# Kernel tuning notes

Hardware: AMD Instinct MI355X
Metric: run time of the kernel (lower is better)

Reference implementation:

```python
import jax, jax.numpy as jnp
import numpy as np


def setup_inputs() -> dict:
    key = jax.random.key(0)
    k1, k2, k3, k4, k5 = jax.random.split(key, 5)
    B, Te, Td, De, Dd = 8, 256, 256, 512, 512
    return {
        "encoder_out_seq": jax.random.normal(k1, (B, Te, De), dtype=jnp.float32),
        "decoder_out_seq": jax.random.normal(k2, (B, Td, Dd), dtype=jnp.float32),
        "W_a": jax.random.normal(k3, (De, De), dtype=jnp.float32) * 0.05,
        "U_a": jax.random.normal(k4, (Dd, De), dtype=jnp.float32) * 0.05,
        "V_a": jax.random.normal(k5, (De, 1), dtype=jnp.float32) * 0.05,
    }


def reference(encoder_out_seq, decoder_out_seq, W_a, U_a, V_a):
    # Bahdanau additive attention, fully vectorized over decoder timesteps
    # (replaces the two sequential K.rnn scans in the original).
    Ws = jnp.einsum('bte,ef->btf', encoder_out_seq, W_a)   # [B,Te,De]
    Uh = jnp.einsum('bqd,df->bqf', decoder_out_seq, U_a)   # [B,Td,De]
    # scores[b,q,t] = tanh(Ws[b,t,:] + Uh[b,q,:]) . V_a
    scores = jnp.einsum('bqtf,f->bqt',
                        jnp.tanh(Ws[:, None, :, :] + Uh[:, :, None, :]),
                        V_a[:, 0])                          # [B,Td,Te]
    e = jax.nn.softmax(scores, axis=-1)                     # attention weights
    c = jnp.einsum('bqt,btf->bqf', e, encoder_out_seq)      # context vectors
    return (c, e)
```

## Files before the change

kernel.cpp:

```cpp
#include <hip/hip_runtime.h>

#define NB 8
#define TE 256
#define TD 256
#define DE 512
#define QT 4

#define K2SCALE 2.8853900817779268f

__global__ __launch_bounds__(512) void gemm2(
    const float* __restrict__ A0, const float* __restrict__ W0, float* __restrict__ C0,
    const float* __restrict__ A1, const float* __restrict__ W1, float* __restrict__ C1)
{
  constexpr int N = DE;
  constexpr int K = DE;
  constexpr int BM = 128, BN = 64, BK = 16;
  constexpr int BMp = BM + 4;
  constexpr int NS = K / BK;
  const float* A = blockIdx.z ? A1 : A0;
  const float* W = blockIdx.z ? W1 : W0;
  float*       C = blockIdx.z ? C1 : C0;
  const int tid = threadIdx.x;
  const int m0 = blockIdx.y * BM;
  const int n0 = blockIdx.x * BN;
  __shared__ __align__(16) float As[2][BK][BMp];
  __shared__ __align__(16) float Bs[2][BK][BN];
  const int am = tid >> 2, ak = (tid & 3) * 4;
  const int bk = tid >> 5, bn = (tid & 31) * 2;
  const int ty = tid >> 4, tx = tid & 15;

  float4 av = *(const float4*)(A + (size_t)(m0 + am) * K + ak);
  float2 bv = *(const float2*)(W + (size_t)bk * N + n0 + bn);
  As[0][ak + 0][am] = av.x; As[0][ak + 1][am] = av.y;
  As[0][ak + 2][am] = av.z; As[0][ak + 3][am] = av.w;
  *(float2*)&Bs[0][bk][bn] = bv;
  __syncthreads();

  float acc[4][4];
  #pragma unroll
  for (int i = 0; i < 4; ++i)
    #pragma unroll
    for (int j = 0; j < 4; ++j) acc[i][j] = 0.f;

  for (int s = 0; s < NS; ++s) {
    const int cur = s & 1;
    if (s + 1 < NS) {
      const int k0 = (s + 1) * BK;
      av = *(const float4*)(A + (size_t)(m0 + am) * K + k0 + ak);
      bv = *(const float2*)(W + (size_t)(k0 + bk) * N + n0 + bn);
    }
    #pragma unroll
    for (int k = 0; k < BK; ++k) {
      float4 a = *(const float4*)&As[cur][k][ty * 4];
      float4 b = *(const float4*)&Bs[cur][k][tx * 4];
      float aa[4] = {a.x, a.y, a.z, a.w};
      float bb[4] = {b.x, b.y, b.z, b.w};
      #pragma unroll
      for (int i = 0; i < 4; ++i)
        #pragma unroll
        for (int j = 0; j < 4; ++j)
          acc[i][j] = fmaf(aa[i], bb[j], acc[i][j]);
    }
    if (s + 1 < NS) {
      const int nxt = cur ^ 1;
      As[nxt][ak + 0][am] = av.x; As[nxt][ak + 1][am] = av.y;
      As[nxt][ak + 2][am] = av.z; As[nxt][ak + 3][am] = av.w;
      *(float2*)&Bs[nxt][bk][bn] = bv;
      __syncthreads();
    }
  }
  #pragma unroll
  for (int i = 0; i < 4; ++i) {
    float4 o = {__builtin_amdgcn_exp2f(acc[i][0] * K2SCALE),
                __builtin_amdgcn_exp2f(acc[i][1] * K2SCALE),
                __builtin_amdgcn_exp2f(acc[i][2] * K2SCALE),
                __builtin_amdgcn_exp2f(acc[i][3] * K2SCALE)};
    *(float4*)(C + (size_t)(m0 + ty * 4 + i) * N + n0 + tx * 4) = o;
  }
}

__global__ __launch_bounds__(512) void attn(
    const float* __restrict__ ws, const float* __restrict__ uh,
    const float* __restrict__ enc, const float* __restrict__ va,
    float* __restrict__ out_c, float* __restrict__ out_e)
{
  const int tid  = threadIdx.x;
  const int wave = tid >> 6;
  const int lane = tid & 63;
  const int b  = blockIdx.x >> 6;
  const int q0 = (blockIdx.x & 63) * QT;
  __shared__ float s_sc[QT][TE];
  __shared__ float red[3][QT][DE];
  const int fbase = lane * 8;

  float4 v0 = *(const float4*)(va + fbase);
  float4 v1 = *(const float4*)(va + fbase + 4);
  float v[8] = {v0.x, v0.y, v0.z, v0.w, v1.x, v1.y, v1.z, v1.w};

  float eu[QT][8];
  #pragma unroll
  for (int q = 0; q < QT; ++q) {
    const float* up = uh + (size_t)(b * TD + q0 + q) * DE + fbase;
    float4 u0 = *(const float4*)(up);
    float4 u1 = *(const float4*)(up + 4);
    eu[q][0] = u0.x; eu[q][1] = u0.y; eu[q][2] = u0.z; eu[q][3] = u0.w;
    eu[q][4] = u1.x; eu[q][5] = u1.y; eu[q][6] = u1.z; eu[q][7] = u1.w;
  }

  const int t0 = wave * 32;
  const float* wp = ws + (size_t)(b * TE + t0) * DE + fbase;
  float4 w0 = *(const float4*)(wp);
  float4 w1 = *(const float4*)(wp + 4);
  for (int t = t0; t < t0 + 32; ++t) {
    float cw[8] = {w0.x, w0.y, w0.z, w0.w, w1.x, w1.y, w1.z, w1.w};
    wp += DE;
    w0 = *(const float4*)(wp);
    w1 = *(const float4*)(wp + 4);
    float a[QT];
    #pragma unroll
    for (int q = 0; q < QT; ++q) {
      float A0 = fmaf(cw[0], eu[q][0], 1.f);
      float A1 = fmaf(cw[1], eu[q][1], 1.f);
      float A2 = fmaf(cw[2], eu[q][2], 1.f);
      float A3 = fmaf(cw[3], eu[q][3], 1.f);
      float B0 = fmaf(cw[4], eu[q][4], 1.f);
      float B1 = fmaf(cw[5], eu[q][5], 1.f);
      float B2 = fmaf(cw[6], eu[q][6], 1.f);
      float B3 = fmaf(cw[7], eu[q][7], 1.f);
      float n1 = fmaf(v[1], A0, v[0] * A1);
      float d1 = A0 * A1;
      float n2 = fmaf(v[3], A2, v[2] * A3);
      float d2 = A2 * A3;
      float N1 = fmaf(n2, d1, n1 * d2);
      float D1 = d1 * d2;
      float n3 = fmaf(v[5], B0, v[4] * B1);
      float d3 = B0 * B1;
      float n4 = fmaf(v[7], B2, v[6] * B3);
      float d4 = B2 * B3;
      float N2 = fmaf(n4, d3, n3 * d4);
      float D2 = d3 * d4;
      float s = N1 * __builtin_amdgcn_rcpf(D1);
      a[q] = fmaf(N2, __builtin_amdgcn_rcpf(D2), s);
    }
    {
      const bool h1 = lane & 1;
      float m0 = h1 ? a[1] : a[0], o0 = h1 ? a[0] : a[1];
      float m1 = h1 ? a[3] : a[2], o1 = h1 ? a[2] : a[3];
      float r0 = m0 + __shfl_xor(o0, 1, 64);
      float r1 = m1 + __shfl_xor(o1, 1, 64);
      const bool h2 = lane & 2;
      float mm = h2 ? r1 : r0, oo = h2 ? r0 : r1;
      float r = mm + __shfl_xor(oo, 2, 64);
      r += __shfl_xor(r, 4, 64);
      r += __shfl_xor(r, 8, 64);
      r += __shfl_xor(r, 16, 64);
      r += __shfl_xor(r, 32, 64);
      if (lane < QT) s_sc[lane][t] = -2.f * r;
    }
  }
  __syncthreads();

  if (wave < QT) {
    const int r = wave;
    float x[4];
    #pragma unroll
    for (int i = 0; i < 4; ++i) x[i] = s_sc[r][lane + 64 * i];
    float m = fmaxf(fmaxf(x[0], x[1]), fmaxf(x[2], x[3]));
    #pragma unroll
    for (int off = 32; off >= 1; off >>= 1) m = fmaxf(m, __shfl_xor(m, off, 64));
    const float L2E = 1.4426950408889634f;
    float ssum = 0.f;
    #pragma unroll
    for (int i = 0; i < 4; ++i) { x[i] = __builtin_amdgcn_exp2f((x[i] - m) * L2E); ssum += x[i]; }
    #pragma unroll
    for (int off = 32; off >= 1; off >>= 1) ssum += __shfl_xor(ssum, off, 64);
    float inv = 1.f / ssum;
    float* oe = out_e + (size_t)(b * TD + q0 + r) * TE;
    #pragma unroll
    for (int i = 0; i < 4; ++i) {
      float e = x[i] * inv;
      s_sc[r][lane + 64 * i] = e;
      oe[lane + 64 * i] = e;
    }
  }
  __syncthreads();

  {
    const int fgrp = tid >> 7;
    const int f4   = (tid & 127) * 4;
    float4 c[QT];
    #pragma unroll
    for (int q = 0; q < QT; ++q) c[q] = make_float4(0.f, 0.f, 0.f, 0.f);
    const float* eb = enc + (size_t)b * TE * DE + f4;
    const int tb = fgrp * 64;
    #pragma unroll 4
    for (int t = tb; t < tb + 64; ++t) {
      float4 ee = *(const float4*)(eb + (size_t)t * DE);
      #pragma unroll
      for (int q = 0; q < QT; ++q) {
        float w = s_sc[q][t];
        c[q].x = fmaf(w, ee.x, c[q].x);
        c[q].y = fmaf(w, ee.y, c[q].y);
        c[q].z = fmaf(w, ee.z, c[q].z);
        c[q].w = fmaf(w, ee.w, c[q].w);
      }
    }
    if (fgrp > 0) {
      #pragma unroll
      for (int q = 0; q < QT; ++q) *(float4*)&red[fgrp - 1][q][f4] = c[q];
    }
    __syncthreads();
    if (fgrp == 0) {
      #pragma unroll
      for (int q = 0; q < QT; ++q) {
        float4 r1 = *(const float4*)&red[0][q][f4];
        float4 r2 = *(const float4*)&red[1][q][f4];
        float4 r3 = *(const float4*)&red[2][q][f4];
        c[q].x += (r1.x + r2.x) + r3.x;
        c[q].y += (r1.y + r2.y) + r3.y;
        c[q].z += (r1.z + r2.z) + r3.z;
        c[q].w += (r1.w + r2.w) + r3.w;
        *(float4*)(out_c + (size_t)(b * TD + q0 + q) * DE + f4) = c[q];
      }
    }
  }
}

extern "C" void kernel_launch(void* const* d_in, const int* in_sizes, int n_in,
                              void* d_out, int out_size, void* d_ws, size_t ws_size,
                              hipStream_t stream) {
  const float* enc = (const float*)d_in[0];
  const float* dec = (const float*)d_in[1];
  const float* Wa  = (const float*)d_in[2];
  const float* Ua  = (const float*)d_in[3];
  const float* Va  = (const float*)d_in[4];
  float* out_c = (float*)d_out;
  float* out_e = out_c + (size_t)NB * TD * DE;
  float* ws = (float*)d_ws;
  float* uh = ws + (size_t)NB * TE * DE;

  gemm2<<<dim3(DE / 64, (NB * TE) / 128, 2), dim3(512), 0, stream>>>(
      enc, Wa, ws, dec, Ua, uh);
  attn<<<dim3(NB * (TD / QT)), dim3(512), 0, stream>>>(
      ws, uh, enc, Va, out_c, out_e);
}
```

Baseline: 80.99 us.

## Replace FP32 SIMT projection GEMM with split-bf16 MFMA GEMM

Replaces the scalar FP32 GEMM that computes both projections with a matrix-core GEMM using bf16x3-style splitting (hi*hi + lo*hi + hi*lo) to keep near-FP32 accuracy. Two new conversion kernels split the activations and weights into bf16 high/low parts, and transpose the weights to a K-contiguous layout. This trades the FMA-bound GEMM for three MFMAs per tile, at the cost of two extra kernel launches and extra memory traffic for the converted operands. The attention kernel is unchanged.

```diff
diff --git a/kernel.cpp b/kernel.cpp
--- a/kernel.cpp
+++ b/kernel.cpp
@@ -8,75 +8,156 @@
 
 #define K2SCALE 2.8853900817779268f
 
-__global__ __launch_bounds__(512) void gemm2(
-    const float* __restrict__ A0, const float* __restrict__ W0, float* __restrict__ C0,
-    const float* __restrict__ A1, const float* __restrict__ W1, float* __restrict__ C1)
+typedef short bf16x8 __attribute__((ext_vector_type(8)));
+typedef float f32x4 __attribute__((ext_vector_type(4)));
+typedef unsigned short u16x8 __attribute__((ext_vector_type(8)));
+
+static __device__ __forceinline__ unsigned short f2bf(float x) {
+  unsigned int u = __float_as_uint(x);
+  u += 0x7fffu + ((u >> 16) & 1u);
+  return (unsigned short)(u >> 16);
+}
+
+__global__ __launch_bounds__(256) void convA(
+    const float* __restrict__ s0, unsigned short* __restrict__ h0, unsigned short* __restrict__ l0,
+    const float* __restrict__ s1, unsigned short* __restrict__ h1, unsigned short* __restrict__ l1)
 {
-  constexpr int N = DE;
-  constexpr int K = DE;
-  constexpr int BM = 128, BN = 64, BK = 16;
-  constexpr int BMp = BM + 4;
-  constexpr int NS = K / BK;
-  const float* A = blockIdx.z ? A1 : A0;
-  const float* W = blockIdx.z ? W1 : W0;
-  float*       C = blockIdx.z ? C1 : C0;
-  const int tid = threadIdx.x;
-  const int m0 = blockIdx.y * BM;
-  const int n0 = blockIdx.x * BN;
-  __shared__ __align__(16) float As[2][BK][BMp];
-  __shared__ __align__(16) float Bs[2][BK][BN];
-  const int am = tid >> 2, ak = (tid & 3) * 4;
-  const int bk = tid >> 5, bn = (tid & 31) * 2;
-  const int ty = tid >> 4, tx = tid & 15;
-
-  float4 av = *(const float4*)(A + (size_t)(m0 + am) * K + ak);
-  float2 bv = *(const float2*)(W + (size_t)bk * N + n0 + bn);
-  As[0][ak + 0][am] = av.x; As[0][ak + 1][am] = av.y;
-  As[0][ak + 2][am] = av.z; As[0][ak + 3][am] = av.w;
-  *(float2*)&Bs[0][bk][bn] = bv;
+  const float* s = blockIdx.z ? s1 : s0;
+  unsigned short* H = blockIdx.z ? h1 : h0;
+  unsigned short* L = blockIdx.z ? l1 : l0;
+  size_t base = ((size_t)blockIdx.x * 256 + threadIdx.x) * 8;
+  float4 x0 = *(const float4*)(s + base);
+  float4 x1 = *(const float4*)(s + base + 4);
+  float xs[8] = {x0.x, x0.y, x0.z, x0.w, x1.x, x1.y, x1.z, x1.w};
+  u16x8 h, l;
+  #pragma unroll
+  for (int j = 0; j < 8; ++j) {
+    unsigned short hh = f2bf(xs[j]);
+    float hf = __uint_as_float((unsigned int)hh << 16);
+    h[j] = hh;
+    l[j] = f2bf(xs[j] - hf);
+  }
+  *(u16x8*)(H + base) = h;
+  *(u16x8*)(L + base) = l;
+}
+
+__global__ __launch_bounds__(256) void convB(
+    const float* __restrict__ w0, unsigned short* __restrict__ h0, unsigned short* __restrict__ l0,
+    const float* __restrict__ w1, unsigned short* __restrict__ h1, unsigned short* __restrict__ l1)
+{
+  const float* W = blockIdx.z ? w1 : w0;
+  unsigned short* H = blockIdx.z ? h1 : h0;
+  unsigned short* L = blockIdx.z ? l1 : l0;
+  __shared__ unsigned short sh[32][33], sl[32][33];
+  const int t = threadIdx.x;
+  const int k0 = blockIdx.y * 32, n0 = blockIdx.x * 32;
+  const int r = t >> 3, c = (t & 7) * 4;
+  float4 x = *(const float4*)(W + (size_t)(k0 + r) * DE + n0 + c);
+  float xs[4] = {x.x, x.y, x.z, x.w};
+  #pragma unroll
+  for (int j = 0; j < 4; ++j) {
+    unsigned short hh = f2bf(xs[j]);
+    float hf = __uint_as_float((unsigned int)hh << 16);
+    sh[r][c + j] = hh;
+    sl[r][c + j] = f2bf(xs[j] - hf);
+  }
   __syncthreads();
-
-  float acc[4][4];
-  #pragma unroll
-  for (int i = 0; i < 4; ++i)
-    #pragma unroll
-    for (int j = 0; j < 4; ++j) acc[i][j] = 0.f;
-
-  for (int s = 0; s < NS; ++s) {
-    const int cur = s & 1;
-    if (s + 1 < NS) {
-      const int k0 = (s + 1) * BK;
-      av = *(const float4*)(A + (size_t)(m0 + am) * K + k0 + ak);
-      bv = *(const float2*)(W + (size_t)(k0 + bk) * N + n0 + bn);
-    }
-    #pragma unroll
-    for (int k = 0; k < BK; ++k) {
-      float4 a = *(const float4*)&As[cur][k][ty * 4];
-      float4 b = *(const float4*)&Bs[cur][k][tx * 4];
-      float aa[4] = {a.x, a.y, a.z, a.w};
-      float bb[4] = {b.x, b.y, b.z, b.w};
-      #pragma unroll
-      for (int i = 0; i < 4; ++i)
-        #pragma unroll
-        for (int j = 0; j < 4; ++j)
-          acc[i][j] = fmaf(aa[i], bb[j], acc[i][j]);
-    }
-    if (s + 1 < NS) {
-      const int nxt = cur ^ 1;
-      As[nxt][ak + 0][am] = av.x; As[nxt][ak + 1][am] = av.y;
-      As[nxt][ak + 2][am] = av.z; As[nxt][ak + 3][am] = av.w;
-      *(float2*)&Bs[nxt][bk][bn] = bv;
-      __syncthreads();
-    }
-  }
-  #pragma unroll
-  for (int i = 0; i < 4; ++i) {
-    float4 o = {__builtin_amdgcn_exp2f(acc[i][0] * K2SCALE),
-                __builtin_amdgcn_exp2f(acc[i][1] * K2SCALE),
-                __builtin_amdgcn_exp2f(acc[i][2] * K2SCALE),
-                __builtin_amdgcn_exp2f(acc[i][3] * K2SCALE)};
-    *(float4*)(C + (size_t)(m0 + ty * 4 + i) * N + n0 + tx * 4) = o;
-  }
+  ushort4 oh, ol;
+  oh.x = sh[c + 0][r]; oh.y = sh[c + 1][r]; oh.z = sh[c + 2][r]; oh.w = sh[c + 3][r];
+  ol.x = sl[c + 0][r]; ol.y = sl[c + 1][r]; ol.z = sl[c + 2][r]; ol.w = sl[c + 3][r];
+  *(ushort4*)(H + (size_t)(n0 + r) * DE + k0 + c) = oh;
+  *(ushort4*)(L + (size_t)(n0 + r) * DE + k0 + c) = ol;
+}
+
+__global__ __launch_bounds__(256) void gemm_mfma(
+    const unsigned short* __restrict__ AH0, const unsigned short* __restrict__ AL0,
+    const unsigned short* __restrict__ BH0, const unsigned short* __restrict__ BL0,
+    float* __restrict__ C0,
+    const unsigned short* __restrict__ AH1, const unsigned short* __restrict__ AL1,
+    const unsigned short* __restrict__ BH1, const unsigned short* __restrict__ BL1,
+    float* __restrict__ C1)
+{
+  const unsigned short* AH = blockIdx.z ? AH1 : AH0;
+  const unsigned short* AL = blockIdx.z ? AL1 : AL0;
+  const unsigned short* BH = blockIdx.z ? BH1 : BH0;
+  const unsigned short* BL = blockIdx.z ? BL1 : BL0;
+  float*               C  = blockIdx.z ? C1  : C0;
+  const int tid  = threadIdx.x;
+  const int lane = tid & 63;
+  const int wave = tid >> 6;
+  const int wm = wave >> 1, wn = wave & 1;
+  const int g = lane >> 4, r16 = lane & 15;
+  const int m0 = blockIdx.y * 128, n0 = blockIdx.x * 64;
+  __shared__ __align__(16) unsigned short Ah[128][40], Al[128][40];
+  __shared__ __align__(16) unsigned short Bh[64][40],  Bl[64][40];
+  const int arow = tid >> 2;
+  const int apart = (tid & 3) * 8;
+
+  u16x8 pa0, pa1, pla0, pla1, pb, plb;
+#define LOADTILE(KT) do {                                                   \
+    const size_t ko = (size_t)(KT) * 32 + apart;                            \
+    const unsigned short* pa_ = AH + (size_t)(m0 + arow) * 512 + ko;        \
+    const unsigned short* pl_ = AL + (size_t)(m0 + arow) * 512 + ko;        \
+    const unsigned short* qb_ = BH + (size_t)(n0 + arow) * 512 + ko;        \
+    const unsigned short* ql_ = BL + (size_t)(n0 + arow) * 512 + ko;        \
+    pa0 = *(const u16x8*)pa_;  pa1 = *(const u16x8*)(pa_ + 64 * 512);       \
+    pla0 = *(const u16x8*)pl_; pla1 = *(const u16x8*)(pl_ + 64 * 512);      \
+    pb = *(const u16x8*)qb_;   plb = *(const u16x8*)ql_;                    \
+  } while (0)
+
+  f32x4 accm[4][2], acce[4][2];
+  #pragma unroll
+  for (int mt = 0; mt < 4; ++mt)
+    #pragma unroll
+    for (int nt = 0; nt < 2; ++nt) {
+      accm[mt][nt] = (f32x4){0.f, 0.f, 0.f, 0.f};
+      acce[mt][nt] = (f32x4){0.f, 0.f, 0.f, 0.f};
+    }
+
+  LOADTILE(0);
+  for (int kt = 0; kt < 16; ++kt) {
+    __syncthreads();
+    *(u16x8*)&Ah[arow][apart] = pa0;
+    *(u16x8*)&Ah[arow + 64][apart] = pa1;
+    *(u16x8*)&Al[arow][apart] = pla0;
+    *(u16x8*)&Al[arow + 64][apart] = pla1;
+    *(u16x8*)&Bh[arow][apart] = pb;
+    *(u16x8*)&Bl[arow][apart] = plb;
+    __syncthreads();
+    if (kt + 1 < 16) LOADTILE(kt + 1);
+    bf16x8 ah[4], al[4], bh[2], bl[2];
+    #pragma unroll
+    for (int mt = 0; mt < 4; ++mt) {
+      ah[mt] = *(const bf16x8*)&Ah[wm * 64 + mt * 16 + r16][g * 8];
+      al[mt] = *(const bf16x8*)&Al[wm * 64 + mt * 16 + r16][g * 8];
+    }
+    #pragma unroll
+    for (int nt = 0; nt < 2; ++nt) {
+      bh[nt] = *(const bf16x8*)&Bh[wn * 32 + nt * 16 + r16][g * 8];
+      bl[nt] = *(const bf16x8*)&Bl[wn * 32 + nt * 16 + r16][g * 8];
+    }
+    #pragma unroll
+    for (int mt = 0; mt < 4; ++mt)
+      #pragma unroll
+      for (int nt = 0; nt < 2; ++nt) {
+        accm[mt][nt] = __builtin_amdgcn_mfma_f32_16x16x32_bf16(ah[mt], bh[nt], accm[mt][nt], 0, 0, 0);
+        acce[mt][nt] = __builtin_amdgcn_mfma_f32_16x16x32_bf16(al[mt], bh[nt], acce[mt][nt], 0, 0, 0);
+        acce[mt][nt] = __builtin_amdgcn_mfma_f32_16x16x32_bf16(ah[mt], bl[nt], acce[mt][nt], 0, 0, 0);
+      }
+  }
+#undef LOADTILE
+
+  #pragma unroll
+  for (int mt = 0; mt < 4; ++mt)
+    #pragma unroll
+    for (int nt = 0; nt < 2; ++nt)
+      #pragma unroll
+      for (int j = 0; j < 4; ++j) {
+        float vsum = accm[mt][nt][j] + acce[mt][nt][j];
+        int row = m0 + wm * 64 + mt * 16 + g * 4 + j;
+        int col = n0 + wn * 32 + nt * 16 + r16;
+        C[(size_t)row * 512 + col] = __builtin_amdgcn_exp2f(vsum * K2SCALE);
+      }
 }
 
 __global__ __launch_bounds__(512) void attn(
@@ -236,11 +317,22 @@
   const float* Va  = (const float*)d_in[4];
   float* out_c = (float*)d_out;
   float* out_e = out_c + (size_t)NB * TD * DE;
+
   float* ws = (float*)d_ws;
-  float* uh = ws + (size_t)NB * TE * DE;
-
-  gemm2<<<dim3(DE / 64, (NB * TE) / 128, 2), dim3(512), 0, stream>>>(
-      enc, Wa, ws, dec, Ua, uh);
+  float* uh = ws + 1048576;
+  unsigned short* AHe = (unsigned short*)(uh + 1048576);
+  unsigned short* ALe = AHe + 1048576;
+  unsigned short* AHd = ALe + 1048576;
+  unsigned short* ALd = AHd + 1048576;
+  unsigned short* BHw = ALd + 1048576;
+  unsigned short* BLw = BHw + 262144;
+  unsigned short* BHu = BLw + 262144;
+  unsigned short* BLu = BHu + 262144;
+
+  convA<<<dim3(512, 1, 2), dim3(256), 0, stream>>>(enc, AHe, ALe, dec, AHd, ALd);
+  convB<<<dim3(16, 16, 2), dim3(256), 0, stream>>>(Wa, BHw, BLw, Ua, BHu, BLu);
+  gemm_mfma<<<dim3(8, 16, 2), dim3(256), 0, stream>>>(
+      AHe, ALe, BHw, BLw, ws, AHd, ALd, BHu, BLu, uh);
   attn<<<dim3(NB * (TD / QT)), dim3(512), 0, stream>>>(
       ws, uh, enc, Va, out_c, out_e);
 }
```

Result: faster. 76.97 us (-5.0%).

## Replace FP32 SIMT GEMM with split-bf16 MFMA GEMM using prepacked operands

Applied to the files above, without the earlier changes.

Adds a prep kernel that splits the encoder/decoder activations and both weight matrices into high and low bf16 parts, stored in an MFMA-fragment layout. A new GEMM does the projections with 16x16x32 bf16 MFMA, three products per tile (hi*hi, lo*hi, hi*lo), to keep near-FP32 accuracy. It also remaps block indices across XCDs and swaps batch/query order in the attention grid. The aim is to move the projection work off FP32 FMA onto matrix cores, at the cost of an extra launch and extra packed-buffer traffic.

```diff
diff --git a/kernel.cpp b/kernel.cpp
--- a/kernel.cpp
+++ b/kernel.cpp
@@ -8,75 +8,152 @@
 
 #define K2SCALE 2.8853900817779268f
 
-__global__ __launch_bounds__(512) void gemm2(
-    const float* __restrict__ A0, const float* __restrict__ W0, float* __restrict__ C0,
-    const float* __restrict__ A1, const float* __restrict__ W1, float* __restrict__ C1)
+typedef short bf16x8 __attribute__((ext_vector_type(8)));
+typedef float f32x4 __attribute__((ext_vector_type(4)));
+typedef unsigned short u16x8 __attribute__((ext_vector_type(8)));
+
+static __device__ __forceinline__ unsigned short f2bf(float x) {
+  unsigned int u = __float_as_uint(x);
+  u += 0x7fffu + ((u >> 16) & 1u);
+  return (unsigned short)(u >> 16);
+}
+
+__global__ __launch_bounds__(256) void prep(
+    const float* __restrict__ enc, const float* __restrict__ dec,
+    const float* __restrict__ Wa,  const float* __restrict__ Ua,
+    unsigned short* __restrict__ AHp, unsigned short* __restrict__ ALp,
+    unsigned short* __restrict__ BHp, unsigned short* __restrict__ BLp)
 {
-  constexpr int N = DE;
-  constexpr int K = DE;
-  constexpr int BM = 128, BN = 64, BK = 16;
-  constexpr int BMp = BM + 4;
-  constexpr int NS = K / BK;
-  const float* A = blockIdx.z ? A1 : A0;
-  const float* W = blockIdx.z ? W1 : W0;
-  float*       C = blockIdx.z ? C1 : C0;
-  const int tid = threadIdx.x;
-  const int m0 = blockIdx.y * BM;
-  const int n0 = blockIdx.x * BN;
-  __shared__ __align__(16) float As[2][BK][BMp];
-  __shared__ __align__(16) float Bs[2][BK][BN];
-  const int am = tid >> 2, ak = (tid & 3) * 4;
-  const int bk = tid >> 5, bn = (tid & 31) * 2;
-  const int ty = tid >> 4, tx = tid & 15;
-
-  float4 av = *(const float4*)(A + (size_t)(m0 + am) * K + ak);
-  float2 bv = *(const float2*)(W + (size_t)bk * N + n0 + bn);
-  As[0][ak + 0][am] = av.x; As[0][ak + 1][am] = av.y;
-  As[0][ak + 2][am] = av.z; As[0][ak + 3][am] = av.w;
-  *(float2*)&Bs[0][bk][bn] = bv;
-  __syncthreads();
-
-  float acc[4][4];
+  const int b = blockIdx.x;
+  const int t = threadIdx.x;
+  if (b < 1024) {
+    const int z  = b >> 9;
+    const int rb = b & 511;
+    const int row = rb * 4 + (t >> 6);
+    const int tk  = t & 63;
+    const int k0  = tk * 8;
+    const float* src = (z ? dec : enc) + (size_t)row * DE + k0;
+    float4 x0 = *(const float4*)(src);
+    float4 x1 = *(const float4*)(src + 4);
+    float xs[8] = {x0.x, x0.y, x0.z, x0.w, x1.x, x1.y, x1.z, x1.w};
+    u16x8 h, l;
+    #pragma unroll
+    for (int j = 0; j < 8; ++j) {
+      unsigned short hh = f2bf(xs[j]);
+      float hf = __uint_as_float((unsigned int)hh << 16);
+      h[j] = hh;
+      l[j] = f2bf(xs[j] - hf);
+    }
+    const int m_tile = row >> 4, r16 = row & 15;
+    const int k_tile = tk >> 2, g = tk & 3;
+    const int lane = g * 16 + r16;
+    const size_t dst = (((size_t)(z * 128 + m_tile) * 16 + k_tile) * 64 + lane) * 8;
+    *(u16x8*)(AHp + dst) = h;
+    *(u16x8*)(ALp + dst) = l;
+  } else {
+    if (t >= 128) return;
+    const int idx = b - 1024;
+    const int z  = idx >> 8;
+    const int ti = idx & 255;
+    const int k0 = (ti >> 4) * 32, n0 = (ti & 15) * 32;
+    const int sub = t >> 6, l = t & 63;
+    const int r16 = l & 15, g = l >> 4;
+    const int n = n0 + sub * 16 + r16;
+    const float* W = z ? Ua : Wa;
+    u16x8 h, lo;
+    #pragma unroll
+    for (int e = 0; e < 8; ++e) {
+      float x = W[(size_t)(k0 + g * 8 + e) * DE + n];
+      unsigned short hh = f2bf(x);
+      float hf = __uint_as_float((unsigned int)hh << 16);
+      h[e] = hh;
+      lo[e] = f2bf(x - hf);
+    }
+    const int n_tile = (ti & 15) * 2 + sub;
+    const int k_tile = ti >> 4;
+    const size_t dst = (((size_t)(z * 32 + n_tile) * 16 + k_tile) * 64 + l) * 8;
+    *(u16x8*)(BHp + dst) = h;
+    *(u16x8*)(BLp + dst) = lo;
+  }
+}
+
+__global__ __launch_bounds__(256) void gemm_pk(
+    const unsigned short* __restrict__ AH, const unsigned short* __restrict__ AL,
+    const unsigned short* __restrict__ BH, const unsigned short* __restrict__ BL,
+    float* __restrict__ C0, float* __restrict__ C1)
+{
+  const int blk = blockIdx.x;
+  const int xcd = blk & 7;
+  const int i   = blk >> 3;
+  const int z   = xcd >> 2;
+  const int mg  = (xcd & 3) * 8 + (i >> 3);
+  const int ng  = i & 7;
+  const int w   = threadIdx.x >> 6;
+  const int lane = threadIdx.x & 63;
+  const int mt2 = mg * 2 + (w >> 1);
+  const int nt2 = ng * 2 + (w & 1);
+  const int mtile0 = mt2 * 2, ntile0 = nt2 * 2;
+
+  const unsigned short* pah = AH + ((size_t)(z * 128 + mtile0) * 16) * 512 + lane * 8;
+  const unsigned short* pal = AL + ((size_t)(z * 128 + mtile0) * 16) * 512 + lane * 8;
+  const unsigned short* pbh = BH + ((size_t)(z * 32 + ntile0) * 16) * 512 + lane * 8;
+  const unsigned short* pbl = BL + ((size_t)(z * 32 + ntile0) * 16) * 512 + lane * 8;
+
+  f32x4 m00 = {0,0,0,0}, m01 = {0,0,0,0}, m10 = {0,0,0,0}, m11 = {0,0,0,0};
+  f32x4 e00 = {0,0,0,0}, e01 = {0,0,0,0}, e10 = {0,0,0,0}, e11 = {0,0,0,0};
+
+  bf16x8 ah0 = *(const bf16x8*)(pah);
+  bf16x8 ah1 = *(const bf16x8*)(pah + 8192);
+  bf16x8 al0 = *(const bf16x8*)(pal);
+  bf16x8 al1 = *(const bf16x8*)(pal + 8192);
+  bf16x8 bh0 = *(const bf16x8*)(pbh);
+  bf16x8 bh1 = *(const bf16x8*)(pbh + 8192);
+  bf16x8 bl0 = *(const bf16x8*)(pbl);
+  bf16x8 bl1 = *(const bf16x8*)(pbl + 8192);
+
+  for (int kt = 0; kt < 16; ++kt) {
+    bf16x8 cah0 = ah0, cah1 = ah1, cal0 = al0, cal1 = al1;
+    bf16x8 cbh0 = bh0, cbh1 = bh1, cbl0 = bl0, cbl1 = bl1;
+    if (kt < 15) {
+      pah += 512; pal += 512; pbh += 512; pbl += 512;
+      ah0 = *(const bf16x8*)(pah);
+      ah1 = *(const bf16x8*)(pah + 8192);
+      al0 = *(const bf16x8*)(pal);
+      al1 = *(const bf16x8*)(pal + 8192);
+      bh0 = *(const bf16x8*)(pbh);
+      bh1 = *(const bf16x8*)(pbh + 8192);
+      bl0 = *(const bf16x8*)(pbl);
+      bl1 = *(const bf16x8*)(pbl + 8192);
+    }
+    m00 = __builtin_amdgcn_mfma_f32_16x16x32_bf16(cah0, cbh0, m00, 0, 0, 0);
+    m01 = __builtin_amdgcn_mfma_f32_16x16x32_bf16(cah0, cbh1, m01, 0, 0, 0);
+    m10 = __builtin_amdgcn_mfma_f32_16x16x32_bf16(cah1, cbh0, m10, 0, 0, 0);
+    m11 = __builtin_amdgcn_mfma_f32_16x16x32_bf16(cah1, cbh1, m11, 0, 0, 0);
+    e00 = __builtin_amdgcn_mfma_f32_16x16x32_bf16(cal0, cbh0, e00, 0, 0, 0);
+    e00 = __builtin_amdgcn_mfma_f32_16x16x32_bf16(cah0, cbl0, e00, 0, 0, 0);
+    e01 = __builtin_amdgcn_mfma_f32_16x16x32_bf16(cal0, cbh1, e01, 0, 0, 0);
+    e01 = __builtin_amdgcn_mfma_f32_16x16x32_bf16(cah0, cbl1, e01, 0, 0, 0);
+    e10 = __builtin_amdgcn_mfma_f32_16x16x32_bf16(cal1, cbh0, e10, 0, 0, 0);
+    e10 = __builtin_amdgcn_mfma_f32_16x16x32_bf16(cah1, cbl0, e10, 0, 0, 0);
+    e11 = __builtin_amdgcn_mfma_f32_16x16x32_bf16(cal1, cbh1, e11, 0, 0, 0);
+    e11 = __builtin_amdgcn_mfma_f32_16x16x32_bf16(cah1, cbl1, e11, 0, 0, 0);
+  }
+
+  float* C = z ? C1 : C0;
+  const int g = lane >> 4, r16 = lane & 15;
+  f32x4 vm[2][2] = {{m00, m01}, {m10, m11}};
+  f32x4 ve[2][2] = {{e00, e01}, {e10, e11}};
   #pragma unroll
-  for (int i = 0; i < 4; ++i)
-    #pragma unroll
-    for (int j = 0; j < 4; ++j) acc[i][j] = 0.f;
-
-  for (int s = 0; s < NS; ++s) {
-    const int cur = s & 1;
-    if (s + 1 < NS) {
-      const int k0 = (s + 1) * BK;
-      av = *(const float4*)(A + (size_t)(m0 + am) * K + k0 + ak);
-      bv = *(const float2*)(W + (size_t)(k0 + bk) * N + n0 + bn);
-    }
-    #pragma unroll
-    for (int k = 0; k < BK; ++k) {
-      float4 a = *(const float4*)&As[cur][k][ty * 4];
-      float4 b = *(const float4*)&Bs[cur][k][tx * 4];
-      float aa[4] = {a.x, a.y, a.z, a.w};
-      float bb[4] = {b.x, b.y, b.z, b.w};
+  for (int mt = 0; mt < 2; ++mt)
+    #pragma unroll
+    for (int nt = 0; nt < 2; ++nt)
       #pragma unroll
-      for (int i = 0; i < 4; ++i)
-        #pragma unroll
-        for (int j = 0; j < 4; ++j)
-          acc[i][j] = fmaf(aa[i], bb[j], acc[i][j]);
-    }
-    if (s + 1 < NS) {
-      const int nxt = cur ^ 1;
-      As[nxt][ak + 0][am] = av.x; As[nxt][ak + 1][am] = av.y;
-      As[nxt][ak + 2][am] = av.z; As[nxt][ak + 3][am] = av.w;
-      *(float2*)&Bs[nxt][bk][bn] = bv;
-      __syncthreads();
-    }
-  }
-  #pragma unroll
-  for (int i = 0; i < 4; ++i) {
-    float4 o = {__builtin_amdgcn_exp2f(acc[i][0] * K2SCALE),
-                __builtin_amdgcn_exp2f(acc[i][1] * K2SCALE),
-                __builtin_amdgcn_exp2f(acc[i][2] * K2SCALE),
-                __builtin_amdgcn_exp2f(acc[i][3] * K2SCALE)};
-    *(float4*)(C + (size_t)(m0 + ty * 4 + i) * N + n0 + tx * 4) = o;
-  }
+      for (int jj = 0; jj < 4; ++jj) {
+        float vsum = vm[mt][nt][jj] + ve[mt][nt][jj];
+        int row = (mtile0 + mt) * 16 + g * 4 + jj;
+        int col = (ntile0 + nt) * 16 + r16;
+        C[(size_t)row * 512 + col] = __builtin_amdgcn_exp2f(vsum * K2SCALE);
+      }
 }
 
 __global__ __launch_bounds__(512) void attn(
@@ -87,8 +164,8 @@
   const int tid  = threadIdx.x;
   const int wave = tid >> 6;
   const int lane = tid & 63;
-  const int b  = blockIdx.x >> 6;
-  const int q0 = (blockIdx.x & 63) * QT;
+  const int b  = blockIdx.x & 7;
+  const int q0 = (blockIdx.x >> 3) * QT;
   __shared__ float s_sc[QT][TE];
   __shared__ float red[3][QT][DE];
   const int fbase = lane * 8;
@@ -236,11 +313,16 @@
   const float* Va  = (const float*)d_in[4];
   float* out_c = (float*)d_out;
   float* out_e = out_c + (size_t)NB * TD * DE;
+
   float* ws = (float*)d_ws;
-  float* uh = ws + (size_t)NB * TE * DE;
-
-  gemm2<<<dim3(DE / 64, (NB * TE) / 128, 2), dim3(512), 0, stream>>>(
-      enc, Wa, ws, dec, Ua, uh);
+  float* uh = ws + 1048576;
+  unsigned short* AHp = (unsigned short*)(uh + 1048576);
+  unsigned short* ALp = AHp + 2097152;
+  unsigned short* BHp = ALp + 2097152;
+  unsigned short* BLp = BHp + 524288;
+
+  prep<<<dim3(1536), dim3(256), 0, stream>>>(enc, dec, Wa, Ua, AHp, ALp, BHp, BLp);
+  gemm_pk<<<dim3(512), dim3(256), 0, stream>>>(AHp, ALp, BHp, BLp, ws, uh);
   attn<<<dim3(NB * (TD / QT)), dim3(512), 0, stream>>>(
       ws, uh, enc, Va, out_c, out_e);
 }
```

Result: faster. 69.96 us (-13.6%).
